# Kernel tuning notes

Measured on AMD Instinct MI355X. Metric: run time of the kernel, lower is better.

## Reference

```python
import math
import jax, jax.numpy as jnp
import numpy as np

PERCENTAGES = [0.004, 0.006, 0.008, 0.01, 0.012]
RADIUS = 1.0          # init kwarg / uniform-loss radius
REPULSION_H = 0.0005  # h in get_repulsion_loss


def pairwise_sqdist(x, y):
    # x: [B,N,3], y: [B,M,3] -> [B,N,M] squared euclidean distances
    d2 = (jnp.sum(x * x, -1)[:, :, None]
          + jnp.sum(y * y, -1)[:, None, :]
          - 2.0 * jnp.einsum('bnd,bmd->bnm', x, y))
    return jnp.maximum(d2, 0.0)


def knn_sqdist(x, k):
    # sorted (ascending) squared distances to k nearest neighbors (incl. self)
    d2 = pairwise_sqdist(x, x)
    neg, _ = jax.lax.top_k(-d2, k)
    return -neg  # [B,N,k]


def fps(pcd, npoint):
    # furthest point sampling, start at index 0 (pn2 convention)
    B, N, _ = pcd.shape
    def step(carry, _):
        dist, last = carry
        p = jnp.take_along_axis(pcd, last[:, None, None], axis=1)  # [B,1,3]
        d = jnp.sum((pcd - p) ** 2, -1)                            # [B,N]
        dist = jnp.minimum(dist, d)
        nxt = jnp.argmax(dist, axis=-1)
        return (dist, nxt), nxt
    idx0 = jnp.zeros((B,), jnp.int32)
    dist0 = jnp.full((B, N), 1e10, pcd.dtype)
    _, rest = jax.lax.scan(step, (dist0, idx0), None, length=npoint - 1)
    return jnp.concatenate([idx0[None], rest], axis=0).T  # [B,npoint]


def ball_query(r, nsample, pcd, centers):
    # pn2 ball_query: first nsample indices with d2 < r^2, padded with first hit
    N = pcd.shape[1]
    d2 = pairwise_sqdist(centers, pcd)                       # [B,S,N]
    cand = jnp.where(d2 < r * r, jnp.arange(N)[None, None, :], N)
    sorted_idx = jnp.sort(cand, axis=-1)[..., :nsample]      # [B,S,nsample]
    first = sorted_idx[..., :1]
    return jnp.where(sorted_idx == N, first, sorted_idx)


def get_cd_loss(pred, gt, pcd_radius):
    d2 = pairwise_sqdist(gt, pred)       # [B,N,M]
    cost_for = jnp.min(d2, axis=2)       # gt -> pred, [B,N]
    cost_bac = jnp.min(d2, axis=1)       # pred -> gt, [B,M]
    cost = 0.8 * cost_for + 0.2 * cost_bac
    cost = cost / pcd_radius
    return jnp.mean(cost)


def get_repulsion_loss(pcd, h=REPULSION_H):
    d2 = knn_sqdist(pcd, 5)[:, :, 1:5]   # squared dists to 4 nearest (excl self)
    return jnp.mean(jnp.maximum(-d2 + h, 0.0))


def get_uniform_loss(pcd, radius=RADIUS):
    B, N, _ = pcd.shape
    npoint = int(N * 0.05)
    fidx = fps(pcd, npoint)
    new_xyz = jnp.take_along_axis(pcd, fidx[:, :, None], axis=1)  # [B,npoint,3]
    loss = 0.0
    for p in PERCENTAGES:
        nsample = int(N * p)
        r = math.sqrt(p * radius)
        disk_area = math.pi * radius ** 2 / N
        expect_len = math.sqrt(disk_area)
        idx = ball_query(r, nsample, pcd, new_xyz)            # [B,npoint,nsample]
        grouped = jax.vmap(lambda pts, i: pts[i])(pcd, idx)   # [B,npoint,nsample,3]
        grouped = grouped.reshape(B, npoint * nsample, 3)     # cat(unbind(dim=1))
        nn_d2 = knn_sqdist(grouped, 2)[:, :, 1:]              # [B,M,1]
        uniform_dist = jnp.abs(jnp.sqrt(nn_d2) + 1e-8)
        uniform_dist = jnp.mean(uniform_dist, axis=1)         # [B,1]
        uniform_dist = (uniform_dist - expect_len) ** 2 / (expect_len + 1e-8)
        loss = loss + jnp.mean(uniform_dist) * (p * 100.0) ** 2
    return loss / len(PERCENTAGES)


def setup_inputs() -> dict:
    key = jax.random.key(0)
    k1, k2 = jax.random.split(key)
    pred = jax.random.normal(k1, (8, 2048, 3), jnp.float32)
    gt = jax.random.normal(k2, (8, 2048, 3), jnp.float32)
    pcd_radius = jnp.ones((1,), jnp.float32)
    return {"pred": pred, "gt": gt, "pcd_radius": pcd_radius}


def reference(pred, gt, pcd_radius):
    cd = get_cd_loss(pred, gt, pcd_radius)
    rep = get_repulsion_loss(pred)
    uni = get_uniform_loss(pred)
    return cd + rep + uni
```

## Files before the change

### kernel.cpp

```cpp
#include <hip/hip_runtime.h>
#include <math.h>

#define BB 8
#define NN 2048
#define NPOINT 102
#define H_REP 0.0005f

typedef float v2f __attribute__((ext_vector_type(2)));

__device__ const int    c_ns[5] = {8, 12, 16, 20, 24};
__device__ const double c_p[5]  = {0.004, 0.006, 0.008, 0.01, 0.012};

#define OFF_CD 0
#define OFF_REP 512
#define OFF_UK 768
#define N_DBL 896

__device__ inline double aload_d(const double* p) {
    return __hip_atomic_load(p, __ATOMIC_RELAXED, __HIP_MEMORY_SCOPE_AGENT);
}

__device__ inline void ins5(float c, float& t0, float& t1, float& t2, float& t3, float& t4) {
    float lo;
    lo = fminf(t0, c); c = fmaxf(t0, c); t0 = lo;
    lo = fminf(t1, c); c = fmaxf(t1, c); t1 = lo;
    lo = fminf(t2, c); c = fmaxf(t2, c); t2 = lo;
    lo = fminf(t3, c); c = fmaxf(t3, c); t3 = lo;
    t4 = fminf(t4, c);
}

union SMemP1 {
    struct { float4 sB[NN]; float pm[4][128]; } cd;
    struct { float4 sP[NN]; float pm[4][64][5]; } rep;
    struct { float4 sl4[2][4]; float slz[2][4]; int sFi[NPOINT]; } fps;
};

__global__ __launch_bounds__(256, 2) void k_phase1(const float* __restrict__ pred,
                                                   const float* __restrict__ gt,
                                                   int* __restrict__ fidx,
                                                   double* __restrict__ part,
                                                   int* __restrict__ done) {
    __shared__ SMemP1 sm;
    int bid = blockIdx.x;
    int tid = threadIdx.x;
    int lane = tid & 63, wid = tid >> 6;

    if (bid == 8 && tid == 0) *done = 0;

    if (bid < 8) {
        __builtin_amdgcn_s_setprio(1);
        int b = bid;
        const float* pp = pred + (size_t)b * NN * 3;
        float px[8], py[8], pz[8], dist[8];
#pragma unroll
        for (int k = 0; k < 8; k++) {
            int i = (wid << 9) + (k << 6) + lane;
            px[k] = pp[i * 3 + 0];
            py[k] = pp[i * 3 + 1];
            pz[k] = pp[i * 3 + 2];
            dist[k] = 1e10f;
        }
        if (tid == 0) sm.fps.sFi[0] = 0;
        float lx = pp[0], ly = pp[1], lz = pp[2];
#pragma unroll 1
        for (int step = 1; step < NPOINT; ++step) {
            float bv = -1.0f;
            int bi = 0;
#pragma unroll
            for (int k = 0; k < 8; k++) {
                float dx = px[k] - lx, dy = py[k] - ly, dz = pz[k] - lz;
                float nd = fminf(dist[k], dx * dx + dy * dy + dz * dz);
                dist[k] = nd;
                bool better = nd > bv;
                bv = better ? nd : bv;
                bi = better ? ((wid << 9) + (k << 6) + lane) : bi;
            }
            {
                float v2; int i2; bool take;
#define DPPC(CTRL)                                                                          \
                v2 = __int_as_float(__builtin_amdgcn_update_dpp(                            \
                        __float_as_int(bv), __float_as_int(bv), CTRL, 0xF, 0xF, false));    \
                i2 = __builtin_amdgcn_update_dpp(bi, bi, CTRL, 0xF, 0xF, false);            \
                take = (v2 > bv) || (v2 == bv && i2 < bi);                                  \
                bv = take ? v2 : bv; bi = take ? i2 : bi;
                DPPC(0x121)
                DPPC(0x122)
                DPPC(0x124)
                DPPC(0x128)
                DPPC(0x142)
                DPPC(0x143)
#undef DPPC
            }
            float wx = 0.f, wy = 0.f, wz = 0.f;
            bool own = false;
#pragma unroll
            for (int k = 0; k < 8; k++) {
                bool m = (bi == ((wid << 9) + (k << 6) + lane));
                wx = m ? px[k] : wx;
                wy = m ? py[k] : wy;
                wz = m ? pz[k] : wz;
                own = own || m;
            }
            int pb = step & 1;
            if (own) {
                sm.fps.sl4[pb][wid] = make_float4(bv, __int_as_float(bi), wx, wy);
                sm.fps.slz[pb][wid] = wz;
            }
            __syncthreads();
            float fv = -2.0f, fx = 0.f, fy = 0.f, fz = 0.f;
            int fi = 0;
#pragma unroll
            for (int w = 0; w < 4; w++) {
                float4 s4 = sm.fps.sl4[pb][w];
                float szv = sm.fps.slz[pb][w];
                int i2 = __float_as_int(s4.y);
                bool take = (s4.x > fv) || (s4.x == fv && i2 < fi);
                fv = take ? s4.x : fv; fi = take ? i2 : fi;
                fx = take ? s4.z : fx; fy = take ? s4.w : fy;
                fz = take ? szv : fz;
            }
            if (tid == 0) sm.fps.sFi[step] = fi;
            lx = fx; ly = fy; lz = fz;
        }
        __syncthreads();
        for (int s = tid; s < NPOINT; s += 256) fidx[b * NPOINT + s] = sm.fps.sFi[s];
    } else if (bid < 264) {
        int r = bid - 8;
        int z = r >> 7;
        int b = (r >> 4) & 7;
        int xb = r & 15;
        const float* A = z ? pred : gt;
        const float* Bp = z ? gt : pred;
        const float* bb = Bp + (size_t)b * NN * 3;
        for (int j = tid; j < NN; j += 256) {
            sm.cd.sB[j] = make_float4(bb[j * 3 + 0], bb[j * 3 + 1], bb[j * 3 + 2], 0.0f);
        }
        int rowA = xb * 128 + lane;
        int rowB = rowA + 64;
        const float* aA = A + ((size_t)b * NN + rowA) * 3;
        const float* aB = A + ((size_t)b * NN + rowB) * 3;
        float axA = aA[0], ayA = aA[1], azA = aA[2];
        float axB = aB[0], ayB = aB[1], azB = aB[2];
        __syncthreads();
        float mnA = 1e30f, mnB = 1e30f;
        int j0 = wid * 512;
#pragma unroll 8
        for (int jj = 0; jj < 512; jj++) {
            float4 p = sm.cd.sB[j0 + jj];
            float dxA = axA - p.x, dyA = ayA - p.y, dzA = azA - p.z;
            mnA = fminf(mnA, dxA * dxA + dyA * dyA + dzA * dzA);
            float dxB = axB - p.x, dyB = ayB - p.y, dzB = azB - p.z;
            mnB = fminf(mnB, dxB * dxB + dyB * dyB + dzB * dzB);
        }
        sm.cd.pm[wid][lane] = mnA;
        sm.cd.pm[wid][64 + lane] = mnB;
        __syncthreads();
        if (tid < 128) {
            double v = (double)fminf(fminf(sm.cd.pm[0][tid], sm.cd.pm[1][tid]),
                                     fminf(sm.cd.pm[2][tid], sm.cd.pm[3][tid]));
            for (int off = 32; off; off >>= 1) v += __shfl_down(v, off, 64);
            if (lane == 0) part[OFF_CD + r * 2 + (tid >> 6)] = v;
        }
    } else {
        int r = bid - 264;
        int b = r >> 5;
        int xb = r & 31;
        const float* pp = pred + (size_t)b * NN * 3;
        for (int j = tid; j < NN; j += 256) {
            sm.rep.sP[j] = make_float4(pp[j * 3 + 0], pp[j * 3 + 1], pp[j * 3 + 2], 0.0f);
        }
        int row = xb * 64 + lane;
        __syncthreads();
        float4 q = sm.rep.sP[row];
        float t0 = 1e30f, t1 = 1e30f, t2 = 1e30f, t3 = 1e30f, t4 = 1e30f;
        int j0 = wid * 512;
#pragma unroll 8
        for (int jj = 0; jj < 512; jj++) {
            float4 p = sm.rep.sP[j0 + jj];
            float dx = q.x - p.x, dy = q.y - p.y, dz = q.z - p.z;
            ins5(dx * dx + dy * dy + dz * dz, t0, t1, t2, t3, t4);
        }
        sm.rep.pm[wid][lane][0] = t0; sm.rep.pm[wid][lane][1] = t1;
        sm.rep.pm[wid][lane][2] = t2; sm.rep.pm[wid][lane][3] = t3;
        sm.rep.pm[wid][lane][4] = t4;
        __syncthreads();
        if (tid < 64) {
            t0 = sm.rep.pm[0][lane][0]; t1 = sm.rep.pm[0][lane][1]; t2 = sm.rep.pm[0][lane][2];
            t3 = sm.rep.pm[0][lane][3]; t4 = sm.rep.pm[0][lane][4];
#pragma unroll
            for (int w = 1; w < 4; w++) {
#pragma unroll
                for (int k = 0; k < 5; k++) ins5(sm.rep.pm[w][lane][k], t0, t1, t2, t3, t4);
            }
            float s = fmaxf(H_REP - t1, 0.f) + fmaxf(H_REP - t2, 0.f) +
                      fmaxf(H_REP - t3, 0.f) + fmaxf(H_REP - t4, 0.f);
            double v = (double)s;
            for (int off = 32; off; off >>= 1) v += __shfl_down(v, off, 64);
            if (tid == 0) part[OFF_REP + r] = v;
        }
    }
}

union UTail {
    struct { float sx[NN], sy[NN], sz[NN]; } st;
    struct { float pm1[16][128], pm2[16][128]; } pm;
};

__global__ __launch_bounds__(1024, 1) void k_tail(const float* __restrict__ pred,
                                                  const int* __restrict__ fidx,
                                                  double* __restrict__ part,
                                                  int* __restrict__ done,
                                                  const float* __restrict__ radius,
                                                  float* __restrict__ out) {
    __shared__ UTail ut;
    __shared__ unsigned short gidxL[2448];
    __shared__ v2f cX[1232], cY[1232], cZ[1232];
    __shared__ int scnt[NPOINT];
    __shared__ int spre[NPOINT + 1];
    __shared__ int lastFlag;
    int grp = blockIdx.x;
    int pi = grp >> 3, b = grp & 7;
    int ns = c_ns[pi];
    int tid = threadIdx.x, lane = tid & 63, wid = tid >> 6;
    const float* pp = pred + (size_t)b * NN * 3;
    double rd = sqrt(c_p[pi]);
    float r2 = (float)(rd * rd);

    for (int t = tid; t < 3 * NN; t += 1024) {
        float v = pp[t];
        int idx = t / 3;
        int comp = t - idx * 3;
        if (comp == 0) ut.st.sx[idx] = v;
        else if (comp == 1) ut.st.sy[idx] = v;
        else ut.st.sz[idx] = v;
    }
    __syncthreads();

    for (int c = wid; c < NPOINT; c += 16) {
        int ci = fidx[b * NPOINT + c];
        float cx = ut.st.sx[ci], cy = ut.st.sy[ci], cz = ut.st.sz[ci];
        float sc = cx * cx + cy * cy + cz * cz;
        int cnt = 0;
#pragma unroll 4
        for (int j0 = 0; j0 < NN; j0 += 64) {
            int j = j0 + lane;
            float x = ut.st.sx[j], y = ut.st.sy[j], z = ut.st.sz[j];
            float sj = x * x + y * y + z * z;
            float d2 = fmaxf(sc + sj - 2.0f * (cx * x + cy * y + cz * z), 0.0f);
            bool prd = d2 < r2;
            unsigned long long mask = __ballot(prd);
            if (prd) {
                int pos = cnt + (int)__popcll(mask & ((1ull << lane) - 1ull));
                if (pos < ns) gidxL[c * ns + pos] = (unsigned short)j;
            }
            cnt += (int)__popcll(mask);
        }
        if (lane == 0) scnt[c] = min(cnt, ns);
    }
    __syncthreads();
    if (tid <= NPOINT) {
        int v = 0;
        if (tid >= 1) {
            int sc_ = scnt[tid - 1];
            v = sc_ | ((sc_ + (sc_ < ns ? 1 : 0)) << 16);
        }
        spre[tid] = v;
    }
    __syncthreads();
    for (int s = 1; s <= NPOINT; s <<= 1) {
        int t = 0;
        if (tid <= NPOINT && tid >= s) t = spre[tid - s];
        __syncthreads();
        if (tid <= NPOINT) spre[tid] += t;
        __syncthreads();
    }
    int Q = spre[NPOINT] & 0xffff;
    int CC = spre[NPOINT] >> 16;
    int CCpad = (CC + 31) & ~31;
    float* fX = (float*)cX; float* fY = (float*)cY; float* fZ = (float*)cZ;
    for (int s = tid; s < CCpad; s += 1024) {
        float x = 1e30f, y = 1e30f, z = 1e30f;
        if (s < CC) {
            int lo = 0, hi = NPOINT - 1;
#pragma unroll
            for (int it = 0; it < 7; ++it) {
                int mid = (lo + hi + 1) >> 1;
                bool ge = ((spre[mid] >> 16) <= s);
                lo = ge ? mid : lo;
                hi = ge ? hi : mid - 1;
            }
            int p = s - (spre[lo] >> 16);
            int dup = (scnt[lo] < ns) ? 1 : 0;
            int id = gidxL[lo * ns + max(0, p - dup)];
            x = ut.st.sx[id]; y = ut.st.sy[id]; z = ut.st.sz[id];
        }
        fX[s] = x; fY[s] = y; fZ[s] = z;
    }
    __syncthreads();
    int CHp = CCpad >> 5;
    int j0p = wid * CHp;
    double racc = 0.0;
    for (int tb = 0; tb < Q; tb += 128) {
        float qx[2], qy[2], qz[2];
        double wgt[2];
#pragma unroll
        for (int hh = 0; hh < 2; hh++) {
            int q = tb + lane + 64 * hh;
            qx[hh] = 0.f; qy[hh] = 0.f; qz[hh] = 0.f; wgt[hh] = 0.0;
            if (q < Q) {
                int lo = 0, hi = NPOINT - 1;
#pragma unroll
                for (int it = 0; it < 7; ++it) {
                    int mid = (lo + hi + 1) >> 1;
                    bool ge = ((spre[mid] & 0xffff) <= q);
                    lo = ge ? mid : lo;
                    hi = ge ? hi : mid - 1;
                }
                int p = q - (spre[lo] & 0xffff);
                int dup = (scnt[lo] < ns) ? 1 : 0;
                int cslot = (spre[lo] >> 16) + (p == 0 ? 0 : p + dup);
                qx[hh] = fX[cslot]; qy[hh] = fY[cslot]; qz[hh] = fZ[cslot];
                wgt[hh] = (p == 0) ? (double)(1 + ns - scnt[lo]) : 1.0;
            }
        }
        v2f qax = {qx[0], qx[0]}, qay = {qy[0], qy[0]}, qaz = {qz[0], qz[0]};
        v2f qbx = {qx[1], qx[1]}, qby = {qy[1], qy[1]}, qbz = {qz[1], qz[1]};
        v2f m1A = {1e30f, 1e30f}, m2A = {1e30f, 1e30f};
        v2f m1B = {1e30f, 1e30f}, m2B = {1e30f, 1e30f};
#pragma unroll 4
        for (int jj = 0; jj < CHp; jj++) {
            v2f X = cX[j0p + jj], Y = cY[j0p + jj], Z = cZ[j0p + jj];
            v2f dxA = qax - X, dyA = qay - Y, dzA = qaz - Z;
            v2f dA = dxA * dxA + dyA * dyA + dzA * dzA;
            float l0 = fminf(m1A.x, dA.x), h0 = fmaxf(m1A.x, dA.x);
            float l1 = fminf(m1A.y, dA.y), h1 = fmaxf(m1A.y, dA.y);
            m1A = (v2f){l0, l1};
            m2A = (v2f){fminf(m2A.x, h0), fminf(m2A.y, h1)};
            v2f dxB = qbx - X, dyB = qby - Y, dzB = qbz - Z;
            v2f dB = dxB * dxB + dyB * dyB + dzB * dzB;
            float l2 = fminf(m1B.x, dB.x), h2 = fmaxf(m1B.x, dB.x);
            float l3 = fminf(m1B.y, dB.y), h3 = fmaxf(m1B.y, dB.y);
            m1B = (v2f){l2, l3};
            m2B = (v2f){fminf(m2B.x, h2), fminf(m2B.y, h3)};
        }
        float a1 = fminf(m1A.x, m1A.y);
        float a2 = fminf(fmaxf(m1A.x, m1A.y), fminf(m2A.x, m2A.y));
        float b1 = fminf(m1B.x, m1B.y);
        float b2 = fminf(fmaxf(m1B.x, m1B.y), fminf(m2B.x, m2B.y));
        ut.pm.pm1[wid][lane] = a1; ut.pm.pm2[wid][lane] = a2;
        ut.pm.pm1[wid][64 + lane] = b1; ut.pm.pm2[wid][64 + lane] = b2;
        __syncthreads();
        if (tid < 128) {
            float c1 = ut.pm.pm1[0][tid], c2 = ut.pm.pm2[0][tid];
#pragma unroll
            for (int w = 1; w < 16; w++) {
                float d1 = ut.pm.pm1[w][tid], d2 = ut.pm.pm2[w][tid];
                float n1 = fminf(c1, d1);
                float n2 = fminf(fmaxf(c1, d1), fminf(c2, d2));
                c1 = n1; c2 = n2;
            }
            int q = tb + tid;
            double v = 0.0;
            if (q < Q) v = wgt[tid >> 6] * (double)(sqrtf(c2) + 1e-8f);
            for (int off = 32; off; off >>= 1) v += __shfl_down(v, off, 64);
            if ((tid & 63) == 0) racc += v;
        }
        __syncthreads();
    }
    if (tid == 0) part[OFF_UK + grp * 2 + 0] = racc;
    if (tid == 64) part[OFF_UK + grp * 2 + 1] = racc;
    __threadfence();
    __syncthreads();
    if (tid == 0) lastFlag = (atomicAdd(done, 1) == 39);
    __syncthreads();
    if (!lastFlag) return;
    __threadfence();
    if (tid >= 64) return;
    double s0 = 0.0, s1 = 0.0, sr = 0.0;
#pragma unroll
    for (int k = 0; k < 4; k++) {
        s0 += aload_d(&part[OFF_CD + lane + 64 * k]);
        s1 += aload_d(&part[OFF_CD + 256 + lane + 64 * k]);
        sr += aload_d(&part[OFF_REP + lane + 64 * k]);
    }
    double v = 0.0;
    if (lane < 40) {
        int pi2 = lane >> 3;
        double m = aload_d(&part[OFF_UK + lane * 2]) + aload_d(&part[OFF_UK + lane * 2 + 1]);
        double p = c_p[pi2];
        int M2 = NPOINT * c_ns[pi2];
        double disk_area = M_PI * 1.0 / (double)NN;
        double e = sqrt(disk_area);
        m = m / (double)M2;
        double d = m - e;
        double w = (p * 100.0) * (p * 100.0);
        v = d * d / (e + 1e-8) * w / 40.0;
    }
    for (int off = 32; off; off >>= 1) {
        v += __shfl_down(v, off, 64);
        s0 += __shfl_down(s0, off, 64);
        s1 += __shfl_down(s1, off, 64);
        sr += __shfl_down(sr, off, 64);
    }
    if (lane == 0) {
        double cd = (0.8 * s0 + 0.2 * s1) / ((double)BB * NN) / (double)radius[0];
        double rep = sr / ((double)BB * NN * 4.0);
        out[0] = (float)(cd + rep + v);
    }
}

extern "C" void kernel_launch(void* const* d_in, const int* in_sizes, int n_in,
                              void* d_out, int out_size, void* d_ws, size_t ws_size,
                              hipStream_t stream) {
    const float* pred = (const float*)d_in[0];
    const float* gt = (const float*)d_in[1];
    const float* radius = (const float*)d_in[2];
    float* out = (float*)d_out;

    double* part = (double*)d_ws;
    int* ints = (int*)(part + N_DBL);
    int* done = ints;
    int* fidx = ints + 16;

    hipLaunchKernelGGL(k_phase1, dim3(520), dim3(256), 0, stream, pred, gt, fidx, part, done);
    hipLaunchKernelGGL(k_tail, dim3(40), dim3(1024), 0, stream, pred, fidx, part, done,
                       radius, out);
}
```

Baseline: 138.6 us.

## Merge phase1 and tail into one persistent kernel with flag-based inter-block sync

Fuses the two kernel launches into a single 560-block kernel. Tail blocks spin-wait on per-batch FPS completion flags, and the last tail block waits for all CD/repulsion blocks before the final reduction. The FPS loop now reads the selected point's coordinates from a shared-memory copy instead of doing an ownership scan. The tail work is moved from 1024-thread blocks to 256-thread blocks, so each wave does more work and the intra-block reduction is shorter. An added memset launch resets the flags, and the spin-waits rely on the producer blocks being co-resident with the waiting blocks.

```diff
diff --git a/kernel.cpp b/kernel.cpp
--- a/kernel.cpp
+++ b/kernel.cpp
@@ -15,7 +15,19 @@
 #define OFF_REP 512
 #define OFF_UK 768
 #define N_DBL 896
-
+#define F_FPS 0
+#define F_DONE2 8
+#define F_UKD 9
+
+__device__ inline int aload(const int* p) {
+    return __hip_atomic_load(p, __ATOMIC_ACQUIRE, __HIP_MEMORY_SCOPE_AGENT);
+}
+__device__ inline void astore(int* p, int v) {
+    __hip_atomic_store(p, v, __ATOMIC_RELEASE, __HIP_MEMORY_SCOPE_AGENT);
+}
+__device__ inline int aiload(const int* p) {
+    return __hip_atomic_load(p, __ATOMIC_RELAXED, __HIP_MEMORY_SCOPE_AGENT);
+}
 __device__ inline double aload_d(const double* p) {
     return __hip_atomic_load(p, __ATOMIC_RELAXED, __HIP_MEMORY_SCOPE_AGENT);
 }
@@ -29,23 +41,32 @@
     t4 = fminf(t4, c);
 }
 
-union SMemP1 {
+union SMemAll {
     struct { float4 sB[NN]; float pm[4][128]; } cd;
     struct { float4 sP[NN]; float pm[4][64][5]; } rep;
-    struct { float4 sl4[2][4]; float slz[2][4]; int sFi[NPOINT]; } fps;
+    struct { float4 sP[NN]; float2 sl[2][4]; int sFi[NPOINT]; } fps;
+    struct {
+        float sx[NN], sy[NN], sz[NN];
+        v2f cX[1232], cY[1232], cZ[1232];
+        float pm1[4][128], pm2[4][128];
+        unsigned short gidxL[2448];
+        int scnt[NPOINT];
+        int spre[NPOINT + 1];
+    } tail;
 };
 
-__global__ __launch_bounds__(256, 2) void k_phase1(const float* __restrict__ pred,
-                                                   const float* __restrict__ gt,
-                                                   int* __restrict__ fidx,
-                                                   double* __restrict__ part,
-                                                   int* __restrict__ done) {
-    __shared__ SMemP1 sm;
+__global__ __launch_bounds__(256, 2) void k_mega(const float* __restrict__ pred,
+                                                 const float* __restrict__ gt,
+                                                 const float* __restrict__ radius,
+                                                 int* __restrict__ fidx,
+                                                 double* __restrict__ part,
+                                                 int* __restrict__ flags,
+                                                 float* __restrict__ out) {
+    __shared__ SMemAll sm;
+    __shared__ int lastFlag;
     int bid = blockIdx.x;
     int tid = threadIdx.x;
     int lane = tid & 63, wid = tid >> 6;
-
-    if (bid == 8 && tid == 0) *done = 0;
 
     if (bid < 8) {
         __builtin_amdgcn_s_setprio(1);
@@ -55,20 +76,21 @@
 #pragma unroll
         for (int k = 0; k < 8; k++) {
             int i = (wid << 9) + (k << 6) + lane;
-            px[k] = pp[i * 3 + 0];
-            py[k] = pp[i * 3 + 1];
-            pz[k] = pp[i * 3 + 2];
-            dist[k] = 1e10f;
+            float x = pp[i * 3 + 0], y = pp[i * 3 + 1], z = pp[i * 3 + 2];
+            px[k] = x; py[k] = y; pz[k] = z; dist[k] = 1e10f;
+            sm.fps.sP[i] = make_float4(x, y, z, 0.0f);
         }
         if (tid == 0) sm.fps.sFi[0] = 0;
-        float lx = pp[0], ly = pp[1], lz = pp[2];
+        __syncthreads();
+        int last = 0;
 #pragma unroll 1
         for (int step = 1; step < NPOINT; ++step) {
+            float4 lp = sm.fps.sP[last];
             float bv = -1.0f;
             int bi = 0;
 #pragma unroll
             for (int k = 0; k < 8; k++) {
-                float dx = px[k] - lx, dy = py[k] - ly, dz = pz[k] - lz;
+                float dx = px[k] - lp.x, dy = py[k] - lp.y, dz = pz[k] - lp.z;
                 float nd = fminf(dist[k], dx * dx + dy * dy + dz * dz);
                 dist[k] = nd;
                 bool better = nd > bv;
@@ -91,39 +113,27 @@
                 DPPC(0x143)
 #undef DPPC
             }
-            float wx = 0.f, wy = 0.f, wz = 0.f;
-            bool own = false;
-#pragma unroll
-            for (int k = 0; k < 8; k++) {
-                bool m = (bi == ((wid << 9) + (k << 6) + lane));
-                wx = m ? px[k] : wx;
-                wy = m ? py[k] : wy;
-                wz = m ? pz[k] : wz;
-                own = own || m;
-            }
             int pb = step & 1;
-            if (own) {
-                sm.fps.sl4[pb][wid] = make_float4(bv, __int_as_float(bi), wx, wy);
-                sm.fps.slz[pb][wid] = wz;
-            }
+            if (lane == 63) sm.fps.sl[pb][wid] = make_float2(bv, __int_as_float(bi));
             __syncthreads();
-            float fv = -2.0f, fx = 0.f, fy = 0.f, fz = 0.f;
+            float fv = -2.0f;
             int fi = 0;
 #pragma unroll
             for (int w = 0; w < 4; w++) {
-                float4 s4 = sm.fps.sl4[pb][w];
-                float szv = sm.fps.slz[pb][w];
-                int i2 = __float_as_int(s4.y);
-                bool take = (s4.x > fv) || (s4.x == fv && i2 < fi);
-                fv = take ? s4.x : fv; fi = take ? i2 : fi;
-                fx = take ? s4.z : fx; fy = take ? s4.w : fy;
-                fz = take ? szv : fz;
+                float2 s = sm.fps.sl[pb][w];
+                int i2 = __float_as_int(s.y);
+                bool take = (s.x > fv) || (s.x == fv && i2 < fi);
+                fv = take ? s.x : fv;
+                fi = take ? i2 : fi;
             }
             if (tid == 0) sm.fps.sFi[step] = fi;
-            lx = fx; ly = fy; lz = fz;
+            last = fi;
         }
         __syncthreads();
         for (int s = tid; s < NPOINT; s += 256) fidx[b * NPOINT + s] = sm.fps.sFi[s];
+        __threadfence();
+        __syncthreads();
+        if (tid == 0) astore(&flags[F_FPS + b], 1);
     } else if (bid < 264) {
         int r = bid - 8;
         int z = r >> 7;
@@ -161,7 +171,10 @@
             for (int off = 32; off; off >>= 1) v += __shfl_down(v, off, 64);
             if (lane == 0) part[OFF_CD + r * 2 + (tid >> 6)] = v;
         }
-    } else {
+        __syncthreads();
+        __threadfence();
+        if (tid == 0) atomicAdd(&flags[F_DONE2], 1);
+    } else if (bid < 520) {
         int r = bid - 264;
         int b = r >> 5;
         int xb = r & 31;
@@ -198,214 +211,206 @@
             for (int off = 32; off; off >>= 1) v += __shfl_down(v, off, 64);
             if (tid == 0) part[OFF_REP + r] = v;
         }
-    }
-}
-
-union UTail {
-    struct { float sx[NN], sy[NN], sz[NN]; } st;
-    struct { float pm1[16][128], pm2[16][128]; } pm;
-};
-
-__global__ __launch_bounds__(1024, 1) void k_tail(const float* __restrict__ pred,
-                                                  const int* __restrict__ fidx,
-                                                  double* __restrict__ part,
-                                                  int* __restrict__ done,
-                                                  const float* __restrict__ radius,
-                                                  float* __restrict__ out) {
-    __shared__ UTail ut;
-    __shared__ unsigned short gidxL[2448];
-    __shared__ v2f cX[1232], cY[1232], cZ[1232];
-    __shared__ int scnt[NPOINT];
-    __shared__ int spre[NPOINT + 1];
-    __shared__ int lastFlag;
-    int grp = blockIdx.x;
-    int pi = grp >> 3, b = grp & 7;
-    int ns = c_ns[pi];
-    int tid = threadIdx.x, lane = tid & 63, wid = tid >> 6;
-    const float* pp = pred + (size_t)b * NN * 3;
-    double rd = sqrt(c_p[pi]);
-    float r2 = (float)(rd * rd);
-
-    for (int t = tid; t < 3 * NN; t += 1024) {
-        float v = pp[t];
-        int idx = t / 3;
-        int comp = t - idx * 3;
-        if (comp == 0) ut.st.sx[idx] = v;
-        else if (comp == 1) ut.st.sy[idx] = v;
-        else ut.st.sz[idx] = v;
-    }
-    __syncthreads();
-
-    for (int c = wid; c < NPOINT; c += 16) {
-        int ci = fidx[b * NPOINT + c];
-        float cx = ut.st.sx[ci], cy = ut.st.sy[ci], cz = ut.st.sz[ci];
-        float sc = cx * cx + cy * cy + cz * cz;
-        int cnt = 0;
+        __syncthreads();
+        __threadfence();
+        if (tid == 0) atomicAdd(&flags[F_DONE2], 1);
+    } else {
+        int grp = bid - 520;
+        int pi = grp >> 3, b = grp & 7;
+        int ns = c_ns[pi];
+        const float* pp = pred + (size_t)b * NN * 3;
+        double rd = sqrt(c_p[pi]);
+        float r2 = (float)(rd * rd);
+        if (tid == 0) {
+            while (aload(&flags[F_FPS + b]) == 0) __builtin_amdgcn_s_sleep(16);
+        }
+        __syncthreads();
+        for (int t = tid; t < 3 * NN; t += 256) {
+            float v = pp[t];
+            int idx = t / 3;
+            int comp = t - idx * 3;
+            if (comp == 0) sm.tail.sx[idx] = v;
+            else if (comp == 1) sm.tail.sy[idx] = v;
+            else sm.tail.sz[idx] = v;
+        }
+        __syncthreads();
+        for (int c = wid; c < NPOINT; c += 4) {
+            int ci = aiload(&fidx[b * NPOINT + c]);
+            float cx = sm.tail.sx[ci], cy = sm.tail.sy[ci], cz = sm.tail.sz[ci];
+            float sc = cx * cx + cy * cy + cz * cz;
+            int cnt = 0;
 #pragma unroll 4
-        for (int j0 = 0; j0 < NN; j0 += 64) {
-            int j = j0 + lane;
-            float x = ut.st.sx[j], y = ut.st.sy[j], z = ut.st.sz[j];
-            float sj = x * x + y * y + z * z;
-            float d2 = fmaxf(sc + sj - 2.0f * (cx * x + cy * y + cz * z), 0.0f);
-            bool prd = d2 < r2;
-            unsigned long long mask = __ballot(prd);
-            if (prd) {
-                int pos = cnt + (int)__popcll(mask & ((1ull << lane) - 1ull));
-                if (pos < ns) gidxL[c * ns + pos] = (unsigned short)j;
-            }
-            cnt += (int)__popcll(mask);
-        }
-        if (lane == 0) scnt[c] = min(cnt, ns);
-    }
-    __syncthreads();
-    if (tid <= NPOINT) {
-        int v = 0;
-        if (tid >= 1) {
-            int sc_ = scnt[tid - 1];
-            v = sc_ | ((sc_ + (sc_ < ns ? 1 : 0)) << 16);
-        }
-        spre[tid] = v;
-    }
-    __syncthreads();
-    for (int s = 1; s <= NPOINT; s <<= 1) {
-        int t = 0;
-        if (tid <= NPOINT && tid >= s) t = spre[tid - s];
-        __syncthreads();
-        if (tid <= NPOINT) spre[tid] += t;
-        __syncthreads();
-    }
-    int Q = spre[NPOINT] & 0xffff;
-    int CC = spre[NPOINT] >> 16;
-    int CCpad = (CC + 31) & ~31;
-    float* fX = (float*)cX; float* fY = (float*)cY; float* fZ = (float*)cZ;
-    for (int s = tid; s < CCpad; s += 1024) {
-        float x = 1e30f, y = 1e30f, z = 1e30f;
-        if (s < CC) {
-            int lo = 0, hi = NPOINT - 1;
-#pragma unroll
-            for (int it = 0; it < 7; ++it) {
-                int mid = (lo + hi + 1) >> 1;
-                bool ge = ((spre[mid] >> 16) <= s);
-                lo = ge ? mid : lo;
-                hi = ge ? hi : mid - 1;
-            }
-            int p = s - (spre[lo] >> 16);
-            int dup = (scnt[lo] < ns) ? 1 : 0;
-            int id = gidxL[lo * ns + max(0, p - dup)];
-            x = ut.st.sx[id]; y = ut.st.sy[id]; z = ut.st.sz[id];
-        }
-        fX[s] = x; fY[s] = y; fZ[s] = z;
-    }
-    __syncthreads();
-    int CHp = CCpad >> 5;
-    int j0p = wid * CHp;
-    double racc = 0.0;
-    for (int tb = 0; tb < Q; tb += 128) {
-        float qx[2], qy[2], qz[2];
-        double wgt[2];
-#pragma unroll
-        for (int hh = 0; hh < 2; hh++) {
-            int q = tb + lane + 64 * hh;
-            qx[hh] = 0.f; qy[hh] = 0.f; qz[hh] = 0.f; wgt[hh] = 0.0;
-            if (q < Q) {
+            for (int j0 = 0; j0 < NN; j0 += 64) {
+                int j = j0 + lane;
+                float x = sm.tail.sx[j], y = sm.tail.sy[j], z = sm.tail.sz[j];
+                float sj = x * x + y * y + z * z;
+                float d2 = fmaxf(sc + sj - 2.0f * (cx * x + cy * y + cz * z), 0.0f);
+                bool prd = d2 < r2;
+                unsigned long long mask = __ballot(prd);
+                if (prd) {
+                    int pos = cnt + (int)__popcll(mask & ((1ull << lane) - 1ull));
+                    if (pos < ns) sm.tail.gidxL[c * ns + pos] = (unsigned short)j;
+                }
+                cnt += (int)__popcll(mask);
+            }
+            if (lane == 0) sm.tail.scnt[c] = min(cnt, ns);
+        }
+        __syncthreads();
+        if (tid <= NPOINT) {
+            int v = 0;
+            if (tid >= 1) {
+                int sc_ = sm.tail.scnt[tid - 1];
+                v = sc_ | ((sc_ + (sc_ < ns ? 1 : 0)) << 16);
+            }
+            sm.tail.spre[tid] = v;
+        }
+        __syncthreads();
+        for (int s = 1; s <= NPOINT; s <<= 1) {
+            int t = 0;
+            if (tid <= NPOINT && tid >= s) t = sm.tail.spre[tid - s];
+            __syncthreads();
+            if (tid <= NPOINT) sm.tail.spre[tid] += t;
+            __syncthreads();
+        }
+        int Q = sm.tail.spre[NPOINT] & 0xffff;
+        int CC = sm.tail.spre[NPOINT] >> 16;
+        int CCpad = (CC + 15) & ~15;
+        float* fX = (float*)sm.tail.cX;
+        float* fY = (float*)sm.tail.cY;
+        float* fZ = (float*)sm.tail.cZ;
+        for (int s = tid; s < CCpad; s += 256) {
+            float x = 1e30f, y = 1e30f, z = 1e30f;
+            if (s < CC) {
                 int lo = 0, hi = NPOINT - 1;
 #pragma unroll
                 for (int it = 0; it < 7; ++it) {
                     int mid = (lo + hi + 1) >> 1;
-                    bool ge = ((spre[mid] & 0xffff) <= q);
+                    bool ge = ((sm.tail.spre[mid] >> 16) <= s);
                     lo = ge ? mid : lo;
                     hi = ge ? hi : mid - 1;
                 }
-                int p = q - (spre[lo] & 0xffff);
-                int dup = (scnt[lo] < ns) ? 1 : 0;
-                int cslot = (spre[lo] >> 16) + (p == 0 ? 0 : p + dup);
-                qx[hh] = fX[cslot]; qy[hh] = fY[cslot]; qz[hh] = fZ[cslot];
-                wgt[hh] = (p == 0) ? (double)(1 + ns - scnt[lo]) : 1.0;
-            }
-        }
-        v2f qax = {qx[0], qx[0]}, qay = {qy[0], qy[0]}, qaz = {qz[0], qz[0]};
-        v2f qbx = {qx[1], qx[1]}, qby = {qy[1], qy[1]}, qbz = {qz[1], qz[1]};
-        v2f m1A = {1e30f, 1e30f}, m2A = {1e30f, 1e30f};
-        v2f m1B = {1e30f, 1e30f}, m2B = {1e30f, 1e30f};
+                int p = s - (sm.tail.spre[lo] >> 16);
+                int dup = (sm.tail.scnt[lo] < ns) ? 1 : 0;
+                int id = sm.tail.gidxL[lo * ns + max(0, p - dup)];
+                x = sm.tail.sx[id]; y = sm.tail.sy[id]; z = sm.tail.sz[id];
+            }
+            fX[s] = x; fY[s] = y; fZ[s] = z;
+        }
+        __syncthreads();
+        int CHp = CCpad >> 3;
+        int j0p = wid * CHp;
+        double racc = 0.0;
+        for (int tb = 0; tb < Q; tb += 128) {
+            float qx[2], qy[2], qz[2];
+            double wgt[2];
+#pragma unroll
+            for (int hh = 0; hh < 2; hh++) {
+                int q = tb + lane + 64 * hh;
+                qx[hh] = 0.f; qy[hh] = 0.f; qz[hh] = 0.f; wgt[hh] = 0.0;
+                if (q < Q) {
+                    int lo = 0, hi = NPOINT - 1;
+#pragma unroll
+                    for (int it = 0; it < 7; ++it) {
+                        int mid = (lo + hi + 1) >> 1;
+                        bool ge = ((sm.tail.spre[mid] & 0xffff) <= q);
+                        lo = ge ? mid : lo;
+                        hi = ge ? hi : mid - 1;
+                    }
+                    int p = q - (sm.tail.spre[lo] & 0xffff);
+                    int dup = (sm.tail.scnt[lo] < ns) ? 1 : 0;
+                    int cslot = (sm.tail.spre[lo] >> 16) + (p == 0 ? 0 : p + dup);
+                    qx[hh] = fX[cslot]; qy[hh] = fY[cslot]; qz[hh] = fZ[cslot];
+                    wgt[hh] = (p == 0) ? (double)(1 + ns - sm.tail.scnt[lo]) : 1.0;
+                }
+            }
+            v2f qax = {qx[0], qx[0]}, qay = {qy[0], qy[0]}, qaz = {qz[0], qz[0]};
+            v2f qbx = {qx[1], qx[1]}, qby = {qy[1], qy[1]}, qbz = {qz[1], qz[1]};
+            v2f m1A = {1e30f, 1e30f}, m2A = {1e30f, 1e30f};
+            v2f m1B = {1e30f, 1e30f}, m2B = {1e30f, 1e30f};
 #pragma unroll 4
-        for (int jj = 0; jj < CHp; jj++) {
-            v2f X = cX[j0p + jj], Y = cY[j0p + jj], Z = cZ[j0p + jj];
-            v2f dxA = qax - X, dyA = qay - Y, dzA = qaz - Z;
-            v2f dA = dxA * dxA + dyA * dyA + dzA * dzA;
-            float l0 = fminf(m1A.x, dA.x), h0 = fmaxf(m1A.x, dA.x);
-            float l1 = fminf(m1A.y, dA.y), h1 = fmaxf(m1A.y, dA.y);
-            m1A = (v2f){l0, l1};
-            m2A = (v2f){fminf(m2A.x, h0), fminf(m2A.y, h1)};
-            v2f dxB = qbx - X, dyB = qby - Y, dzB = qbz - Z;
-            v2f dB = dxB * dxB + dyB * dyB + dzB * dzB;
-            float l2 = fminf(m1B.x, dB.x), h2 = fmaxf(m1B.x, dB.x);
-            float l3 = fminf(m1B.y, dB.y), h3 = fmaxf(m1B.y, dB.y);
-            m1B = (v2f){l2, l3};
-            m2B = (v2f){fminf(m2B.x, h2), fminf(m2B.y, h3)};
-        }
-        float a1 = fminf(m1A.x, m1A.y);
-        float a2 = fminf(fmaxf(m1A.x, m1A.y), fminf(m2A.x, m2A.y));
-        float b1 = fminf(m1B.x, m1B.y);
-        float b2 = fminf(fmaxf(m1B.x, m1B.y), fminf(m2B.x, m2B.y));
-        ut.pm.pm1[wid][lane] = a1; ut.pm.pm2[wid][lane] = a2;
-        ut.pm.pm1[wid][64 + lane] = b1; ut.pm.pm2[wid][64 + lane] = b2;
-        __syncthreads();
-        if (tid < 128) {
-            float c1 = ut.pm.pm1[0][tid], c2 = ut.pm.pm2[0][tid];
-#pragma unroll
-            for (int w = 1; w < 16; w++) {
-                float d1 = ut.pm.pm1[w][tid], d2 = ut.pm.pm2[w][tid];
-                float n1 = fminf(c1, d1);
-                float n2 = fminf(fmaxf(c1, d1), fminf(c2, d2));
-                c1 = n1; c2 = n2;
-            }
-            int q = tb + tid;
-            double v = 0.0;
-            if (q < Q) v = wgt[tid >> 6] * (double)(sqrtf(c2) + 1e-8f);
-            for (int off = 32; off; off >>= 1) v += __shfl_down(v, off, 64);
-            if ((tid & 63) == 0) racc += v;
-        }
-        __syncthreads();
-    }
-    if (tid == 0) part[OFF_UK + grp * 2 + 0] = racc;
-    if (tid == 64) part[OFF_UK + grp * 2 + 1] = racc;
-    __threadfence();
-    __syncthreads();
-    if (tid == 0) lastFlag = (atomicAdd(done, 1) == 39);
-    __syncthreads();
-    if (!lastFlag) return;
-    __threadfence();
-    if (tid >= 64) return;
-    double s0 = 0.0, s1 = 0.0, sr = 0.0;
-#pragma unroll
-    for (int k = 0; k < 4; k++) {
-        s0 += aload_d(&part[OFF_CD + lane + 64 * k]);
-        s1 += aload_d(&part[OFF_CD + 256 + lane + 64 * k]);
-        sr += aload_d(&part[OFF_REP + lane + 64 * k]);
-    }
-    double v = 0.0;
-    if (lane < 40) {
-        int pi2 = lane >> 3;
-        double m = aload_d(&part[OFF_UK + lane * 2]) + aload_d(&part[OFF_UK + lane * 2 + 1]);
-        double p = c_p[pi2];
-        int M2 = NPOINT * c_ns[pi2];
-        double disk_area = M_PI * 1.0 / (double)NN;
-        double e = sqrt(disk_area);
-        m = m / (double)M2;
-        double d = m - e;
-        double w = (p * 100.0) * (p * 100.0);
-        v = d * d / (e + 1e-8) * w / 40.0;
-    }
-    for (int off = 32; off; off >>= 1) {
-        v += __shfl_down(v, off, 64);
-        s0 += __shfl_down(s0, off, 64);
-        s1 += __shfl_down(s1, off, 64);
-        sr += __shfl_down(sr, off, 64);
-    }
-    if (lane == 0) {
-        double cd = (0.8 * s0 + 0.2 * s1) / ((double)BB * NN) / (double)radius[0];
-        double rep = sr / ((double)BB * NN * 4.0);
-        out[0] = (float)(cd + rep + v);
+            for (int jj = 0; jj < CHp; jj++) {
+                v2f X = sm.tail.cX[j0p + jj], Y = sm.tail.cY[j0p + jj], Z = sm.tail.cZ[j0p + jj];
+                v2f dxA = qax - X, dyA = qay - Y, dzA = qaz - Z;
+                v2f dA = dxA * dxA + dyA * dyA + dzA * dzA;
+                float l0 = fminf(m1A.x, dA.x), h0 = fmaxf(m1A.x, dA.x);
+                float l1 = fminf(m1A.y, dA.y), h1 = fmaxf(m1A.y, dA.y);
+                m1A = (v2f){l0, l1};
+                m2A = (v2f){fminf(m2A.x, h0), fminf(m2A.y, h1)};
+                v2f dxB = qbx - X, dyB = qby - Y, dzB = qbz - Z;
+                v2f dB = dxB * dxB + dyB * dyB + dzB * dzB;
+                float l2 = fminf(m1B.x, dB.x), h2 = fmaxf(m1B.x, dB.x);
+                float l3 = fminf(m1B.y, dB.y), h3 = fmaxf(m1B.y, dB.y);
+                m1B = (v2f){l2, l3};
+                m2B = (v2f){fminf(m2B.x, h2), fminf(m2B.y, h3)};
+            }
+            float a1 = fminf(m1A.x, m1A.y);
+            float a2 = fminf(fmaxf(m1A.x, m1A.y), fminf(m2A.x, m2A.y));
+            float b1 = fminf(m1B.x, m1B.y);
+            float b2 = fminf(fmaxf(m1B.x, m1B.y), fminf(m2B.x, m2B.y));
+            sm.tail.pm1[wid][lane] = a1; sm.tail.pm2[wid][lane] = a2;
+            sm.tail.pm1[wid][64 + lane] = b1; sm.tail.pm2[wid][64 + lane] = b2;
+            __syncthreads();
+            if (tid < 128) {
+                float c1 = sm.tail.pm1[0][tid], c2 = sm.tail.pm2[0][tid];
+#pragma unroll
+                for (int w = 1; w < 4; w++) {
+                    float d1 = sm.tail.pm1[w][tid], d2 = sm.tail.pm2[w][tid];
+                    float n1 = fminf(c1, d1);
+                    float n2 = fminf(fmaxf(c1, d1), fminf(c2, d2));
+                    c1 = n1; c2 = n2;
+                }
+                int q = tb + tid;
+                double v = 0.0;
+                if (q < Q) v = wgt[tid >> 6] * (double)(sqrtf(c2) + 1e-8f);
+                for (int off = 32; off; off >>= 1) v += __shfl_down(v, off, 64);
+                if ((tid & 63) == 0) racc += v;
+            }
+            __syncthreads();
+        }
+        if (tid == 0) part[OFF_UK + grp * 2 + 0] = racc;
+        if (tid == 64) part[OFF_UK + grp * 2 + 1] = racc;
+        __threadfence();
+        __syncthreads();
+        if (tid == 0) lastFlag = (atomicAdd(&flags[F_UKD], 1) == 39);
+        __syncthreads();
+        if (!lastFlag) return;
+        if (tid == 0) {
+            while (aload(&flags[F_DONE2]) < 512) __builtin_amdgcn_s_sleep(8);
+        }
+        __syncthreads();
+        if (tid >= 64) return;
+        double s0 = 0.0, s1 = 0.0, sr = 0.0;
+#pragma unroll
+        for (int k = 0; k < 4; k++) {
+            s0 += aload_d(&part[OFF_CD + lane + 64 * k]);
+            s1 += aload_d(&part[OFF_CD + 256 + lane + 64 * k]);
+            sr += aload_d(&part[OFF_REP + lane + 64 * k]);
+        }
+        double v = 0.0;
+        if (lane < 40) {
+            int pi2 = lane >> 3;
+            double m = aload_d(&part[OFF_UK + lane * 2]) +
+                       aload_d(&part[OFF_UK + lane * 2 + 1]);
+            double p = c_p[pi2];
+            int M2 = NPOINT * c_ns[pi2];
+            double disk_area = M_PI * 1.0 / (double)NN;
+            double e = sqrt(disk_area);
+            m = m / (double)M2;
+            double d = m - e;
+            double w = (p * 100.0) * (p * 100.0);
+            v = d * d / (e + 1e-8) * w / 40.0;
+        }
+        for (int off = 32; off; off >>= 1) {
+            v += __shfl_down(v, off, 64);
+            s0 += __shfl_down(s0, off, 64);
+            s1 += __shfl_down(s1, off, 64);
+            sr += __shfl_down(sr, off, 64);
+        }
+        if (lane == 0) {
+            double cd = (0.8 * s0 + 0.2 * s1) / ((double)BB * NN) / (double)radius[0];
+            double rep = sr / ((double)BB * NN * 4.0);
+            out[0] = (float)(cd + rep + v);
+        }
     }
 }
 
@@ -418,11 +423,10 @@
     float* out = (float*)d_out;
 
     double* part = (double*)d_ws;
-    int* ints = (int*)(part + N_DBL);
-    int* done = ints;
-    int* fidx = ints + 16;
-
-    hipLaunchKernelGGL(k_phase1, dim3(520), dim3(256), 0, stream, pred, gt, fidx, part, done);
-    hipLaunchKernelGGL(k_tail, dim3(40), dim3(1024), 0, stream, pred, fidx, part, done,
-                       radius, out);
-}
+    int* flags = (int*)(part + N_DBL);
+    int* fidx = flags + 16;
+
+    hipMemsetAsync(flags, 0, 16 * sizeof(int), stream);
+    hipLaunchKernelGGL(k_mega, dim3(560), dim3(256), 0, stream,
+                       pred, gt, radius, fidx, part, flags, out);
+}
```

Result: slower. 171.3 us (+23.6%).
